# Performance work log

Measured on AMD Instinct MI355X. Metric: run time of the kernel, lower is better.

Reference implementation:

```python
import jax, jax.numpy as jnp
import numpy as np
import math

N_HEAD = 16
ROPE_BASE = 10000.0

def _rope_cos_sin(seq_len, head_dim, dtype):
    inv_freq = 1.0 / (ROPE_BASE ** (jnp.arange(0, head_dim, 2, dtype=jnp.float32) / head_dim))
    t = jnp.arange(seq_len, dtype=jnp.float32)
    freqs = t[:, None] * inv_freq[None, :]            # [S, D/2]
    emb = jnp.concatenate([freqs, freqs], axis=-1)     # [S, D]
    # broadcast shape [1, 1, S, D] to match q/k [B, H, S, D]
    return jnp.cos(emb)[None, None].astype(dtype), jnp.sin(emb)[None, None].astype(dtype)

def _rotate_half(x):
    x1, x2 = jnp.split(x, 2, axis=-1)
    return jnp.concatenate([-x2, x1], axis=-1)

def setup_inputs() -> dict:
    key = jax.random.key(0)
    ks = jax.random.split(key, 5)
    B, S, E = 2, 2048, 1024
    x = jax.random.normal(ks[0], (B, S, E), dtype=jnp.float32)
    init = 1.0 / math.sqrt(E)
    Wq = jax.random.normal(ks[1], (E, E), dtype=jnp.float32) * init
    Wk = jax.random.normal(ks[2], (E, E), dtype=jnp.float32) * init
    Wv = jax.random.normal(ks[3], (E, E), dtype=jnp.float32) * init
    Wo = jax.random.normal(ks[4], (E, E), dtype=jnp.float32) * init
    # causal mask: True = masked (masked_fill with -inf)
    attn_mask = jnp.triu(jnp.ones((S, S), dtype=bool), k=1)
    return {"x": x, "Wq": Wq, "Wk": Wk, "Wv": Wv, "Wo": Wo, "attn_mask": attn_mask}

def reference(x, Wq, Wk, Wv, Wo, attn_mask):
    B, S, E = x.shape
    H = N_HEAD
    D = E // H
    # projections (torch Linear: y = x @ W.T), split heads -> [B, H, S, D]
    def proj(W):
        return jnp.einsum('bse,fe->bsf', x, W).reshape(B, S, H, D).transpose(0, 2, 1, 3)
    q, k, v = proj(Wq), proj(Wk), proj(Wv)
    cos, sin = _rope_cos_sin(S, D, x.dtype)
    q = q * cos + _rotate_half(q) * sin
    k = k * cos + _rotate_half(k) * sin
    scale = 1.0 / math.sqrt(D)
    scores = jnp.einsum('bhqd,bhkd->bhqk', q, k) * scale  # [B, H, S, S]
    scores = jnp.where(attn_mask[None, None], -jnp.inf, scores)
    attn = jax.nn.softmax(scores, axis=-1)
    out = jnp.einsum('bhqk,bhkd->bhqd', attn, v)           # [B, H, S, D]
    out = out.transpose(0, 2, 1, 3).reshape(B, S, E)
    return jnp.einsum('bse,fe->bsf', out, Wo)
```

## Files before the change

### kernel.cpp

```cpp
#include <hip/hip_runtime.h>
#include <hip/hip_bf16.h>

#define NB 2
#define NH 16
#define SEQ 2048
#define HD 64
#define EMB 1024

typedef unsigned short u16;
typedef unsigned int u32;
typedef __attribute__((ext_vector_type(8))) short bf16x8;
typedef __attribute__((ext_vector_type(4))) float f32x4;
typedef __attribute__((ext_vector_type(8))) unsigned short us8;

__device__ __forceinline__ float b2f(u16 u) {
    union { unsigned int i; float f; } v; v.i = ((unsigned int)u) << 16; return v.f;
}
__device__ __forceinline__ u16 f2b(float f) {
    union { float f; unsigned int i; } v; v.f = f;
    unsigned int x = v.i;
    return (u16)((x + 0x7FFFu + ((x >> 16) & 1u)) >> 16);
}
__device__ __forceinline__ u32 pk2(float a, float b) {
    union { __hip_bfloat162 h; u32 u; } v;
    v.h = __float22bfloat162_rn(make_float2(a, b));
    return v.u;
}

__device__ __forceinline__ void gld16(const u16* g, u16* l) {
    __builtin_amdgcn_global_load_lds((const __attribute__((address_space(1))) void*)g,
                                     (__attribute__((address_space(3))) void*)l, 16, 0, 0);
}

__device__ __forceinline__ void conv8(const void* src, u16* dst, int i, int isbf16) {
    if (isbf16) {
        *reinterpret_cast<uint4*>(dst + i) =
            *reinterpret_cast<const uint4*>((const u16*)src + i);
    } else {
        const float* s = (const float*)src + i;
        float4 a = *reinterpret_cast<const float4*>(s);
        float4 b = *reinterpret_cast<const float4*>(s + 4);
        us8 v;
        v[0] = f2b(a.x); v[1] = f2b(a.y); v[2] = f2b(a.z); v[3] = f2b(a.w);
        v[4] = f2b(b.x); v[5] = f2b(b.y); v[6] = f2b(b.z); v[7] = f2b(b.w);
        *reinterpret_cast<us8*>(dst + i) = v;
    }
}

__global__ __launch_bounds__(256)
void prep_54571854463007(const void* __restrict__ x,
                         const void* __restrict__ w0, const void* __restrict__ w1,
                         const void* __restrict__ w2, const void* __restrict__ w3,
                         u16* __restrict__ xb, u16* __restrict__ dqkv,
                         u16* __restrict__ dob, int* __restrict__ flag) {
    __shared__ int cnt;
    if (threadIdx.x == 0) cnt = 0;
    __syncthreads();
    const u16 v = ((const u16*)x)[threadIdx.x];
    const int e = (v >> 7) & 0xFF;
    if (e >= 110 && e <= 135) atomicAdd(&cnt, 1);
    __syncthreads();
    const int isbf16 = (cnt >= 200) ? 1 : 0;
    const int blk = blockIdx.x;
    if (blk == 0 && threadIdx.x == 0) *flag = isbf16;
    const int NXB = (NB * SEQ * EMB) / 2048;
    if (blk < NXB) {
        conv8(x, xb, (blk * 256 + threadIdx.x) * 8, isbf16);
    } else {
        const int r = blk - NXB;
        const int seg = r >> 9;
        const int NW = EMB * EMB;
        const void* src = (seg == 0) ? w0 : (seg == 1) ? w1 : (seg == 2) ? w2 : w3;
        u16* dst = (seg < 3) ? (dqkv + (size_t)seg * NW) : dob;
        conv8(src, dst, ((r & 511) * 256 + threadIdx.x) * 8, isbf16);
    }
}

template<int OUT_MODE>
__global__ __launch_bounds__(256)
void gemm_mfma_54571854463007(const u16* __restrict__ A, const u16* __restrict__ Bw,
                              void* __restrict__ C, const int* __restrict__ flagp,
                              int M, int N, int K) {
    __shared__ __align__(16) u16 As[128 * 32];
    __shared__ __align__(16) u16 Bs[128 * 32];
    const int tid  = threadIdx.x;
    const int wave = tid >> 6, lane = tid & 63;
    const int quad = lane >> 4, fr = lane & 15;
    const int wr = (wave >> 1) * 64, wc = (wave & 1) * 64;
    const int m0 = blockIdx.y * 128, n0 = blockIdx.x * 128;
    const int r0 = tid >> 2;
    const int kc = (tid & 3) * 8;
    const f32x4 zz = {0.f, 0.f, 0.f, 0.f};
    f32x4 acc[4][4];
#pragma unroll
    for (int i = 0; i < 4; ++i)
#pragma unroll
        for (int j = 0; j < 4; ++j) acc[i][j] = zz;

    for (int k0 = 0; k0 < K; k0 += 32) {
        gld16(A  + (size_t)(m0 + r0) * K + k0 + kc,      &As[wave * 512]);
        gld16(A  + (size_t)(m0 + 64 + r0) * K + k0 + kc, &As[2048 + wave * 512]);
        gld16(Bw + (size_t)(n0 + r0) * K + k0 + kc,      &Bs[wave * 512]);
        gld16(Bw + (size_t)(n0 + 64 + r0) * K + k0 + kc, &Bs[2048 + wave * 512]);
        __syncthreads();
        bf16x8 af[4], bfr[4];
#pragma unroll
        for (int mi = 0; mi < 4; ++mi)
            af[mi] = *reinterpret_cast<const bf16x8*>(&As[(wr + mi * 16 + fr) * 32 + quad * 8]);
#pragma unroll
        for (int ni = 0; ni < 4; ++ni)
            bfr[ni] = *reinterpret_cast<const bf16x8*>(&Bs[(wc + ni * 16 + fr) * 32 + quad * 8]);
#pragma unroll
        for (int mi = 0; mi < 4; ++mi)
#pragma unroll
            for (int ni = 0; ni < 4; ++ni)
                acc[mi][ni] = __builtin_amdgcn_mfma_f32_16x16x32_bf16(af[mi], bfr[ni], acc[mi][ni], 0, 0, 0);
        __syncthreads();
    }

    if (OUT_MODE == 1) {
        const int t0 = n0 >> 10;
        if (t0 == 0) {
            const float SCL = 0.18033688011112042f;
#pragma unroll
            for (int mi = 0; mi < 4; ++mi)
#pragma unroll
                for (int ni = 0; ni < 4; ++ni)
#pragma unroll
                    for (int r = 0; r < 4; ++r) acc[mi][ni][r] *= SCL;
        }
        if (t0 < 2) {
            const float inv0 = __powf(10000.f, -(float)fr / 32.f);
            const float inv1 = __powf(10000.f, -(float)(fr + 16) / 32.f);
#pragma unroll
            for (int mi = 0; mi < 4; ++mi)
#pragma unroll
                for (int r = 0; r < 4; ++r) {
                    const int s = (m0 + wr + mi * 16 + quad * 4 + r) & (SEQ - 1);
#pragma unroll
                    for (int nl = 0; nl < 2; ++nl) {
                        float sn, cs;
                        __sincosf((float)s * (nl ? inv1 : inv0), &sn, &cs);
                        const float lo = acc[mi][nl][r], hi = acc[mi][nl + 2][r];
                        acc[mi][nl][r]     = lo * cs - hi * sn;
                        acc[mi][nl + 2][r] = hi * cs + lo * sn;
                    }
                }
        }
    }

    const int isbf16 = (OUT_MODE == 0) ? *flagp : 0;
    const size_t TS = (size_t)NB * NH * SEQ * HD;
#pragma unroll
    for (int mi = 0; mi < 4; ++mi)
#pragma unroll
        for (int ni = 0; ni < 4; ++ni)
#pragma unroll
            for (int r = 0; r < 4; ++r) {
                const int m = m0 + wr + mi * 16 + quad * 4 + r;
                const int n = n0 + wc + ni * 16 + fr;
                const float v = acc[mi][ni][r];
                if (OUT_MODE == 1) {
                    const int t = n >> 10, idx = n & 1023;
                    const int h = idx >> 6, d = idx & 63;
                    const int b = m >> 11, s = m & (SEQ - 1);
                    ((u16*)C)[t * TS + ((((size_t)b * NH + h) * SEQ + s) << 6) + d] = f2b(v);
                } else {
                    if (isbf16) ((u16*)C)[(size_t)m * N + n] = f2b(v);
                    else        ((float*)C)[(size_t)m * N + n] = v;
                }
            }
}

__global__ __launch_bounds__(256, 4)
void flash_54571854463007(const u16* __restrict__ Q, const u16* __restrict__ K,
                          const u16* __restrict__ V, u16* __restrict__ AO) {
    __shared__ __align__(16) u16 Kt[2 * 4096];
    __shared__ __align__(16) u16 Vt[2 * 4608];
    const int tid  = threadIdx.x;
    const int w    = tid >> 6, lane = tid & 63;
    const int quad = lane >> 4, fr = lane & 15;
    const int lin = blockIdx.x;
    const int xcd = lin & 7;
    const int p   = lin >> 3;
    const int qt  = 31 - (p >> 2);
    const int bh  = xcd * 4 + (p & 3);
    const int h = bh & 15, b = bh >> 4;
    const size_t base = ((size_t)b * NH + h) * SEQ * HD;
    const int k2   = (tid & 31) * 2;
    const int key0 = (k2 & 3) * 16 + (k2 >> 2);
    const int d8   = ((tid >> 5) & 7) * 8;
    const int total = qt + 1;

    const int krs = lane >> 3;
    const int kch = ((lane & 7) ^ krs) * 8;
    const int swz = fr & 7;
    const int co0 = (quad ^ swz) * 8;
    const int co1 = ((quad + 4) ^ swz) * 8;

    const bf16x8 ones = {(short)0x3F80, (short)0x3F80, (short)0x3F80, (short)0x3F80,
                         (short)0x3F80, (short)0x3F80, (short)0x3F80, (short)0x3F80};

    const u16* qp = Q + base + (size_t)(qt * 64 + w * 16 + fr) * HD + quad * 8;
    const bf16x8 aq0 = *reinterpret_cast<const bf16x8*>(qp);
    const bf16x8 aq1 = *reinterpret_cast<const bf16x8*>(qp + 32);

    {
        const u16* Kg = K + base;
        gld16(Kg + (size_t)((w * 2 + 0) * 8 + krs) * HD + kch, &Kt[(w * 2 + 0) * 512]);
        gld16(Kg + (size_t)((w * 2 + 1) * 8 + krs) * HD + kch, &Kt[(w * 2 + 1) * 512]);
    }
    us8 vc0, vc1, vn0, vn1;
    {
        const u16* vs = V + base + (size_t)key0 * HD + d8;
        vc0 = *reinterpret_cast<const us8*>(vs);
        vc1 = *reinterpret_cast<const us8*>(vs + 16 * HD);
    }

    const f32x4 zz = {0.f, 0.f, 0.f, 0.f};
    f32x4 lacc = zz;
    f32x4 oacc[4];
#pragma unroll
    for (int nt = 0; nt < 4; ++nt) oacc[nt] = zz;

    for (int j = 0; j < total; ++j) {
        const int buf = j & 1;
        const int vb  = buf * 4608;
        const int kb  = buf * 4096;
#pragma unroll
        for (int jj = 0; jj < 8; ++jj) {
            const u32 pk = ((u32)(u16)vc1[jj] << 16) | (u32)(u16)vc0[jj];
            *reinterpret_cast<u32*>(&Vt[vb + (d8 + jj) * 72 + k2]) = pk;
        }
        __syncthreads();
        if (j + 1 < total) {
            const u16* Kg = K + base + (size_t)(j + 1) * 64 * HD;
            const int kb1 = (buf ^ 1) * 4096;
            gld16(Kg + (size_t)((w * 2 + 0) * 8 + krs) * HD + kch, &Kt[kb1 + (w * 2 + 0) * 512]);
            gld16(Kg + (size_t)((w * 2 + 1) * 8 + krs) * HD + kch, &Kt[kb1 + (w * 2 + 1) * 512]);
            const u16* vs = V + base + (size_t)((j + 1) * 64 + key0) * HD + d8;
            vn0 = *reinterpret_cast<const us8*>(vs);
            vn1 = *reinterpret_cast<const us8*>(vs + 16 * HD);
        }
        f32x4 sa[4];
        __builtin_amdgcn_s_setprio(1);
#pragma unroll
        for (int nt = 0; nt < 4; ++nt) {
            const int rb = kb + (nt * 16 + fr) * 64;
            const bf16x8 ka0 = *reinterpret_cast<const bf16x8*>(&Kt[rb + co0]);
            const bf16x8 ka1 = *reinterpret_cast<const bf16x8*>(&Kt[rb + co1]);
            sa[nt] = __builtin_amdgcn_mfma_f32_16x16x32_bf16(ka0, aq0, zz, 0, 0, 0);
            sa[nt] = __builtin_amdgcn_mfma_f32_16x16x32_bf16(ka1, aq1, sa[nt], 0, 0, 0);
        }
        __builtin_amdgcn_s_setprio(0);
        if (j == qt) {
#pragma unroll
            for (int nt = 0; nt < 4; ++nt)
#pragma unroll
                for (int r = 0; r < 4; ++r)
                    if (nt * 16 + quad * 4 + r > w * 16 + fr) sa[nt][r] = -__builtin_inff();
        }
        u32 c01[4], c23[4];
#pragma unroll
        for (int r = 0; r < 4; ++r) {
            c01[r] = pk2(exp2f(sa[0][r]), exp2f(sa[1][r]));
            c23[r] = pk2(exp2f(sa[2][r]), exp2f(sa[3][r]));
        }
        union { u32 u[4]; bf16x8 v; } P0, P1;
        {
            auto a = __builtin_amdgcn_permlane16_swap(c01[0], c01[2], false, false);
            auto bsw = __builtin_amdgcn_permlane32_swap(a[0], a[1], false, false);
            P0.u[0] = (u32)bsw[0]; P1.u[0] = (u32)bsw[1];
        }
        {
            auto a = __builtin_amdgcn_permlane16_swap(c23[0], c23[2], false, false);
            auto bsw = __builtin_amdgcn_permlane32_swap(a[0], a[1], false, false);
            P0.u[1] = (u32)bsw[0]; P1.u[1] = (u32)bsw[1];
        }
        {
            auto a = __builtin_amdgcn_permlane16_swap(c01[1], c01[3], false, false);
            auto bsw = __builtin_amdgcn_permlane32_swap(a[0], a[1], false, false);
            P0.u[2] = (u32)bsw[0]; P1.u[2] = (u32)bsw[1];
        }
        {
            auto a = __builtin_amdgcn_permlane16_swap(c23[1], c23[3], false, false);
            auto bsw = __builtin_amdgcn_permlane32_swap(a[0], a[1], false, false);
            P0.u[3] = (u32)bsw[0]; P1.u[3] = (u32)bsw[1];
        }
        const bf16x8 pa0 = P0.v;
        const bf16x8 pa1 = P1.v;
        __builtin_amdgcn_s_setprio(1);
        lacc = __builtin_amdgcn_mfma_f32_16x16x32_bf16(pa0, ones, lacc, 0, 0, 0);
        lacc = __builtin_amdgcn_mfma_f32_16x16x32_bf16(pa1, ones, lacc, 0, 0, 0);
#pragma unroll
        for (int nt = 0; nt < 4; ++nt) {
            const bf16x8 bv0 = *reinterpret_cast<const bf16x8*>(&Vt[vb + (nt * 16 + fr) * 72 + quad * 8]);
            const bf16x8 bv1 = *reinterpret_cast<const bf16x8*>(&Vt[vb + (nt * 16 + fr) * 72 + 32 + quad * 8]);
            oacc[nt] = __builtin_amdgcn_mfma_f32_16x16x32_bf16(pa0, bv0, oacc[nt], 0, 0, 0);
            oacc[nt] = __builtin_amdgcn_mfma_f32_16x16x32_bf16(pa1, bv1, oacc[nt], 0, 0, 0);
        }
        __builtin_amdgcn_s_setprio(0);
        vc0 = vn0; vc1 = vn1;
    }
#pragma unroll
    for (int r = 0; r < 4; ++r) {
        const float inv = 1.0f / lacc[r];
        const int q = qt * 64 + w * 16 + quad * 4 + r;
#pragma unroll
        for (int nt = 0; nt < 4; ++nt)
            AO[(((size_t)b * SEQ + q) * NH + h) * HD + nt * 16 + fr] = f2b(oacc[nt][r] * inv);
    }
}

extern "C" void kernel_launch(void* const* d_in, const int* in_sizes, int n_in,
                              void* d_out, int out_size, void* d_ws, size_t ws_size,
                              hipStream_t stream) {
    (void)in_sizes; (void)n_in; (void)out_size; (void)ws_size;
    const void* x  = d_in[0];
    const void* Wq = d_in[1];
    const void* Wk = d_in[2];
    const void* Wv = d_in[3];
    const void* Wo = d_in[4];

    char* ws = (char*)d_ws;
    const size_t MB = 1024 * 1024;
    int* flag = (int*)ws;
    u16* xb   = (u16*)(ws + 64);
    u16* Wqkv = (u16*)(ws + 64 + 8 * MB);
    u16* Wob  = (u16*)(ws + 64 + 14 * MB);
    u16* Qb   = (u16*)(ws + 64 + 16 * MB);
    u16* Kb   = (u16*)(ws + 64 + 24 * MB);
    u16* Vb   = (u16*)(ws + 64 + 32 * MB);
    u16* AO   = xb;

    prep_54571854463007<<<dim3(4096), 256, 0, stream>>>(
        x, Wq, Wk, Wv, Wo, xb, Wqkv, Wob, flag);

    const int M = NB * SEQ;
    gemm_mfma_54571854463007<1><<<dim3(3 * EMB / 128, M / 128), 256, 0, stream>>>(
        xb, Wqkv, Qb, flag, M, 3 * EMB, EMB);

    flash_54571854463007<<<dim3(1024), 256, 0, stream>>>(Qb, Kb, Vb, AO);

    gemm_mfma_54571854463007<0><<<dim3(EMB / 128, M / 128), 256, 0, stream>>>(
        AO, Wob, d_out, flag, M, EMB, EMB);
}
```

Baseline: 205.2 us.

## Split long causal query tiles across two KV halves with a combine kernel

```diff
diff --git a/kernel.cpp b/kernel.cpp
--- a/kernel.cpp
+++ b/kernel.cpp
@@ -174,7 +174,9 @@
 
 __global__ __launch_bounds__(256, 4)
 void flash_54571854463007(const u16* __restrict__ Q, const u16* __restrict__ K,
-                          const u16* __restrict__ V, u16* __restrict__ AO) {
+                          const u16* __restrict__ V, u16* __restrict__ AO,
+                          float* __restrict__ OP0, float* __restrict__ OP1,
+                          float* __restrict__ LP0, float* __restrict__ LP1) {
     __shared__ __align__(16) u16 Kt[2 * 4096];
     __shared__ __align__(16) u16 Vt[2 * 4608];
     const int tid  = threadIdx.x;
@@ -182,15 +184,24 @@
     const int quad = lane >> 4, fr = lane & 15;
     const int lin = blockIdx.x;
     const int xcd = lin & 7;
-    const int p   = lin >> 3;
-    const int qt  = 31 - (p >> 2);
-    const int bh  = xcd * 4 + (p & 3);
+    const int r_  = lin >> 3;
+    const int b4  = r_ & 3;
+    const int ti  = r_ >> 2;
+    int qt, kt0, kt1;
+    if (ti < 17)       { qt = 15 + ti; kt0 = 0;  kt1 = 15; }
+    else if (ti == 17) { qt = 31;      kt0 = 16; kt1 = 31; }
+    else {
+        const int g = ti - 18, s = 15 - (g >> 1);
+        if (g & 1) { qt = s + 15; kt0 = 16; kt1 = qt; }
+        else       { qt = s - 1;  kt0 = 0;  kt1 = qt; }
+    }
+    const int bh = xcd * 4 + b4;
+    const bool partial = (qt >= 16);
     const int h = bh & 15, b = bh >> 4;
     const size_t base = ((size_t)b * NH + h) * SEQ * HD;
     const int k2   = (tid & 31) * 2;
     const int key0 = (k2 & 3) * 16 + (k2 >> 2);
     const int d8   = ((tid >> 5) & 7) * 8;
-    const int total = qt + 1;
 
     const int krs = lane >> 3;
     const int kch = ((lane & 7) ^ krs) * 8;
@@ -206,13 +217,13 @@
     const bf16x8 aq1 = *reinterpret_cast<const bf16x8*>(qp + 32);
 
     {
-        const u16* Kg = K + base;
+        const u16* Kg = K + base + (size_t)kt0 * 64 * HD;
         gld16(Kg + (size_t)((w * 2 + 0) * 8 + krs) * HD + kch, &Kt[(w * 2 + 0) * 512]);
         gld16(Kg + (size_t)((w * 2 + 1) * 8 + krs) * HD + kch, &Kt[(w * 2 + 1) * 512]);
     }
     us8 vc0, vc1, vn0, vn1;
     {
-        const u16* vs = V + base + (size_t)key0 * HD + d8;
+        const u16* vs = V + base + (size_t)(kt0 * 64 + key0) * HD + d8;
         vc0 = *reinterpret_cast<const us8*>(vs);
         vc1 = *reinterpret_cast<const us8*>(vs + 16 * HD);
     }
@@ -223,8 +234,8 @@
 #pragma unroll
     for (int nt = 0; nt < 4; ++nt) oacc[nt] = zz;
 
-    for (int j = 0; j < total; ++j) {
-        const int buf = j & 1;
+    for (int kt = kt0; kt <= kt1; ++kt) {
+        const int buf = (kt - kt0) & 1;
         const int vb  = buf * 4608;
         const int kb  = buf * 4096;
 #pragma unroll
@@ -233,12 +244,12 @@
             *reinterpret_cast<u32*>(&Vt[vb + (d8 + jj) * 72 + k2]) = pk;
         }
         __syncthreads();
-        if (j + 1 < total) {
-            const u16* Kg = K + base + (size_t)(j + 1) * 64 * HD;
+        if (kt + 1 <= kt1) {
+            const u16* Kg = K + base + (size_t)(kt + 1) * 64 * HD;
             const int kb1 = (buf ^ 1) * 4096;
             gld16(Kg + (size_t)((w * 2 + 0) * 8 + krs) * HD + kch, &Kt[kb1 + (w * 2 + 0) * 512]);
             gld16(Kg + (size_t)((w * 2 + 1) * 8 + krs) * HD + kch, &Kt[kb1 + (w * 2 + 1) * 512]);
-            const u16* vs = V + base + (size_t)((j + 1) * 64 + key0) * HD + d8;
+            const u16* vs = V + base + (size_t)((kt + 1) * 64 + key0) * HD + d8;
             vn0 = *reinterpret_cast<const us8*>(vs);
             vn1 = *reinterpret_cast<const us8*>(vs + 16 * HD);
         }
@@ -253,7 +264,7 @@
             sa[nt] = __builtin_amdgcn_mfma_f32_16x16x32_bf16(ka1, aq1, sa[nt], 0, 0, 0);
         }
         __builtin_amdgcn_s_setprio(0);
-        if (j == qt) {
+        if (kt == qt) {
 #pragma unroll
             for (int nt = 0; nt < 4; ++nt)
 #pragma unroll
@@ -302,14 +313,52 @@
         __builtin_amdgcn_s_setprio(0);
         vc0 = vn0; vc1 = vn1;
     }
-#pragma unroll
-    for (int r = 0; r < 4; ++r) {
-        const float inv = 1.0f / lacc[r];
-        const int q = qt * 64 + w * 16 + quad * 4 + r;
-#pragma unroll
-        for (int nt = 0; nt < 4; ++nt)
-            AO[(((size_t)b * SEQ + q) * NH + h) * HD + nt * 16 + fr] = f2b(oacc[nt][r] * inv);
-    }
+    if (!partial) {
+#pragma unroll
+        for (int r = 0; r < 4; ++r) {
+            const float inv = 1.0f / lacc[r];
+            const int q = qt * 64 + w * 16 + quad * 4 + r;
+#pragma unroll
+            for (int nt = 0; nt < 4; ++nt)
+                AO[(((size_t)b * SEQ + q) * NH + h) * HD + nt * 16 + fr] = f2b(oacc[nt][r] * inv);
+        }
+    } else {
+        float* OP = (kt0 == 16) ? OP1 : OP0;
+        float* LP = (kt0 == 16) ? LP1 : LP0;
+        const int tb = (bh * 16 + (qt - 16)) * 64;
+#pragma unroll
+        for (int r = 0; r < 4; ++r) {
+            const int qrow = w * 16 + quad * 4 + r;
+            LP[tb + qrow] = lacc[r];
+#pragma unroll
+            for (int nt = 0; nt < 4; ++nt)
+                OP[(size_t)(tb + qrow) * 64 + nt * 16 + fr] = oacc[nt][r];
+        }
+    }
+}
+
+__global__ __launch_bounds__(256)
+void combine_54571854463007(const float* __restrict__ OP0, const float* __restrict__ OP1,
+                            const float* __restrict__ LP0, const float* __restrict__ LP1,
+                            u16* __restrict__ AO) {
+    const int idx  = blockIdx.x * 256 + threadIdx.x;
+    const int row  = idx >> 3;
+    const int d8   = (idx & 7) * 8;
+    const int bh   = row >> 10;
+    const int tile = (row >> 6) & 15;
+    const int qrow = row & 63;
+    const int h = bh & 15, b = bh >> 4;
+    const int q = (16 + tile) * 64 + qrow;
+    const float4* A = reinterpret_cast<const float4*>(&OP0[(size_t)row * 64 + d8]);
+    const float4* Bp = reinterpret_cast<const float4*>(&OP1[(size_t)row * 64 + d8]);
+    const float4 a0 = A[0], a1 = A[1], b0 = Bp[0], b1 = Bp[1];
+    const float inv = 1.0f / (LP0[row] + LP1[row]);
+    us8 o;
+    o[0] = f2b((a0.x + b0.x) * inv); o[1] = f2b((a0.y + b0.y) * inv);
+    o[2] = f2b((a0.z + b0.z) * inv); o[3] = f2b((a0.w + b0.w) * inv);
+    o[4] = f2b((a1.x + b1.x) * inv); o[5] = f2b((a1.y + b1.y) * inv);
+    o[6] = f2b((a1.z + b1.z) * inv); o[7] = f2b((a1.w + b1.w) * inv);
+    *reinterpret_cast<us8*>(&AO[(((size_t)b * SEQ + q) * NH + h) * HD + d8]) = o;
 }
 
 extern "C" void kernel_launch(void* const* d_in, const int* in_sizes, int n_in,
@@ -331,6 +380,10 @@
     u16* Qb   = (u16*)(ws + 64 + 16 * MB);
     u16* Kb   = (u16*)(ws + 64 + 24 * MB);
     u16* Vb   = (u16*)(ws + 64 + 32 * MB);
+    float* OP0 = (float*)(ws + 64 + 40 * MB);
+    float* OP1 = (float*)(ws + 64 + 48 * MB);
+    float* LP0 = (float*)(ws + 64 + 56 * MB);
+    float* LP1 = (float*)(ws + 64 + 56 * MB + 256 * 1024);
     u16* AO   = xb;
 
     prep_54571854463007<<<dim3(4096), 256, 0, stream>>>(
@@ -340,7 +393,9 @@
     gemm_mfma_54571854463007<1><<<dim3(3 * EMB / 128, M / 128), 256, 0, stream>>>(
         xb, Wqkv, Qb, flag, M, 3 * EMB, EMB);
 
-    flash_54571854463007<<<dim3(1024), 256, 0, stream>>>(Qb, Kb, Vb, AO);
+    flash_54571854463007<<<dim3(1536), 256, 0, stream>>>(Qb, Kb, Vb, AO,
+                                                         OP0, OP1, LP0, LP1);
+    combine_54571854463007<<<dim3(1024), 256, 0, stream>>>(OP0, OP1, LP0, LP1, AO);
 
     gemm_mfma_54571854463007<0><<<dim3(EMB / 128, M / 128), 256, 0, stream>>>(
         AO, Wob, d_out, flag, M, EMB, EMB);
```

Result: no change. 204.9 us (-0.2%).
